# Kernel optimization log

Measured on AMD Instinct MI355X. Metric: run time of the kernel, lower is better.

## Reference

```python
import jax, jax.numpy as jnp
import numpy as np

N = 100_000      # nodes
E = 1_200_000    # edges (before self-loops)
F_IN = 128       # num_node_features
G = 256          # number of graphs in the batch
C = 10           # num_classes
NEG_SLOPE = 0.2  # PyG GATConv default


def setup_inputs() -> dict:
    key = jax.random.key(0)
    ks = jax.random.split(key, 20)
    x = jax.random.normal(ks[0], (N, F_IN), jnp.float32)
    edge_index = jax.random.randint(ks[1], (2, E), 0, N, dtype=jnp.int32)
    # sorted graph assignment covering all G graphs (no empty segments)
    batch = (jnp.arange(N, dtype=jnp.int32) * G) // N

    def lin(k, fi, fo):
        return jax.random.normal(k, (fi, fo), jnp.float32) * (1.0 / np.sqrt(fi))

    dims = [(F_IN, 16), (16, 32), (32, 64)]
    params = {}
    for i, (fi, fo) in enumerate(dims, start=1):
        params[f"W{i}"] = lin(ks[3 * i], fi, fo)
        params[f"a{i}_src"] = jax.random.normal(ks[3 * i + 1], (fo,), jnp.float32) * 0.1
        params[f"a{i}_dst"] = jax.random.normal(ks[3 * i + 2], (fo,), jnp.float32) * 0.1
        params[f"b{i}"] = jnp.zeros((fo,), jnp.float32)
    params["fc_w"] = lin(ks[15], 64, C)
    params["fc_b"] = jnp.zeros((C,), jnp.float32)
    return {"x": x, "edge_index": edge_index, "batch": batch, **params}


def _gat_layer(x, src, dst, W, a_src, a_dst, b):
    # h = Theta x; e_ij = LeakyReLU(a_src.h_j + a_dst.h_i), softmax over dst i
    h = x @ W                                     # [N, F]
    s = h @ a_src                                 # [N]
    d = h @ a_dst                                 # [N]
    logits = jax.nn.leaky_relu(s[src] + d[dst], NEG_SLOPE)   # [E+N]
    m = jax.ops.segment_max(logits, dst, num_segments=N)     # per-dst max
    ex = jnp.exp(logits - m[dst])
    denom = jax.ops.segment_sum(ex, dst, num_segments=N)
    alpha = ex / (denom[dst] + 1e-16)             # [E+N]
    out = jax.ops.segment_sum(alpha[:, None] * h[src], dst, num_segments=N)
    return out + b


def reference(x, edge_index, batch, W1, a1_src, a1_dst, b1, W2, a2_src, a2_dst, b2,
              W3, a3_src, a3_dst, b3, fc_w, fc_b):
    # add self-loops (PyG GATConv default) -> every dst segment non-empty
    loops = jnp.arange(N, dtype=edge_index.dtype)
    src = jnp.concatenate([edge_index[0], loops])
    dst = jnp.concatenate([edge_index[1], loops])

    h = jax.nn.relu(_gat_layer(x, src, dst, W1, a1_src, a1_dst, b1))
    # F.dropout(training=False) is a no-op in eval
    h = jax.nn.relu(_gat_layer(h, src, dst, W2, a2_src, a2_dst, b2))
    h = jax.nn.relu(_gat_layer(h, src, dst, W3, a3_src, a3_dst, b3))
    pooled = jax.ops.segment_max(h, batch, num_segments=G)   # global_max_pool [G, 64]
    logits = pooled @ fc_w + fc_b
    return jax.nn.log_softmax(logits, axis=1)
```

## Files before the change

kernel.cpp:

```cpp
#include <hip/hip_runtime.h>
#include <hip/hip_bf16.h>
#include <hip/hip_fp16.h>
#include <math.h>

#define NEG_SLOPE 0.2f
#define NCHUNK 1024
#define BSHIFT 8
#define BNODES 256

__device__ __forceinline__ float leaky(float x) { return x > 0.f ? x : NEG_SLOPE * x; }
__device__ __forceinline__ int usan(int v, int n) { return ((unsigned)v < (unsigned)n) ? v : 0; }

__global__ void chunk_hist(const int* __restrict__ dst, int E, int Ec, int nbuck,
                           int* __restrict__ hmatT) {
    extern __shared__ int hist[];
    int c = blockIdx.x;
    for (int b = threadIdx.x; b < nbuck; b += 256) hist[b] = 0;
    __syncthreads();
    int lo = c * Ec, hi = min(E, lo + Ec);
    for (int e = lo + threadIdx.x; e < hi; e += 256) atomicAdd(&hist[dst[e] >> BSHIFT], 1);
    __syncthreads();
    for (int b = threadIdx.x; b < nbuck; b += 256) hmatT[b * NCHUNK + c] = hist[b];
}

__global__ void mat_scan(int* __restrict__ hmatT, int* __restrict__ btot) {
    __shared__ int wsum[4];
    int b = blockIdx.x;
    int t = threadIdx.x;
    int lane = t & 63, wave = t >> 6;
    int base = b * NCHUNK + t * 4;
    int a0 = hmatT[base], a1 = hmatT[base + 1], a2 = hmatT[base + 2], a3 = hmatT[base + 3];
    int ts = a0 + a1 + a2 + a3;
    int incl = ts;
#pragma unroll
    for (int o = 1; o < 64; o <<= 1) {
        int v = __shfl_up(incl, o);
        if (lane >= o) incl += v;
    }
    if (lane == 63) wsum[wave] = incl;
    __syncthreads();
    int wadd = 0;
#pragma unroll
    for (int w = 0; w < 4; w++) if (w < wave) wadd += wsum[w];
    int excl = wadd + incl - ts;
    hmatT[base] = excl;
    hmatT[base + 1] = excl + a0;
    hmatT[base + 2] = excl + a0 + a1;
    hmatT[base + 3] = excl + a0 + a1 + a2;
    if (t == 255) btot[b] = wadd + incl;
}

__global__ void base_scan(const int* __restrict__ btot, int nbuck, int* __restrict__ bbase,
                          int* __restrict__ offs, int N, int E) {
    __shared__ int wsum[8];
    int t = threadIdx.x;
    int lane = t & 63, wave = t >> 6;
    int v = (t < nbuck) ? btot[t] : 0;
    int incl = v;
#pragma unroll
    for (int o = 1; o < 64; o <<= 1) {
        int s = __shfl_up(incl, o);
        if (lane >= o) incl += s;
    }
    if (lane == 63) wsum[wave] = incl;
    __syncthreads();
    int wadd = 0;
#pragma unroll
    for (int w = 0; w < 8; w++) if (w < wave) wadd += wsum[w];
    incl += wadd;
    if (t <= nbuck) bbase[t] = incl - v;
    if (t == 0) offs[N] = N + E;
}

__global__ void chunk_scatter(const int* __restrict__ src, const int* __restrict__ dst,
                              int E, int Ec, int nbuck, const int* __restrict__ hmatT,
                              const int* __restrict__ bbase, int* __restrict__ bbuf) {
    extern __shared__ int cur[];
    int c = blockIdx.x;
    for (int b = threadIdx.x; b < nbuck; b += 256) cur[b] = bbase[b] + hmatT[b * NCHUNK + c];
    __syncthreads();
    int lo = c * Ec, hi = min(E, lo + Ec);
    for (int e = lo + threadIdx.x; e < hi; e += 256) {
        int d = dst[e];
        int b = d >> BSHIFT;
        int p = atomicAdd(&cur[b], 1);
        bbuf[p] = (src[e] << BSHIFT) | (d & (BNODES - 1));
    }
}

__global__ void bucket_build(const int* __restrict__ bbase, const int* __restrict__ bbuf,
                             int N, int* __restrict__ offs, int* __restrict__ csr) {
    __shared__ int hist[BNODES];
    __shared__ int offl[BNODES];
    __shared__ int cur[BNODES];
    __shared__ int wsum[4];
    int b = blockIdx.x;
    int t = threadIdx.x;
    int lane = t & 63, wave = t >> 6;
    hist[t] = 0;
    __syncthreads();
    int lo = bbase[b], hi = bbase[b + 1];
    for (int j = lo + t; j < hi; j += BNODES) atomicAdd(&hist[bbuf[j] & (BNODES - 1)], 1);
    __syncthreads();
    int own = hist[t];
    int incl = own;
#pragma unroll
    for (int o = 1; o < 64; o <<= 1) {
        int s = __shfl_up(incl, o);
        if (lane >= o) incl += s;
    }
    if (lane == 63) wsum[wave] = incl;
    __syncthreads();
    int wadd = 0;
#pragma unroll
    for (int w = 0; w < 4; w++) if (w < wave) wadd += wsum[w];
    int excl = wadd + incl - own;
    int n = (b << BSHIFT) + t;
    int off_n = n + bbase[b] + excl;
    offl[t] = off_n;
    cur[t] = 0;
    if (n < N) {
        offs[n] = off_n;
        csr[off_n] = n;
    }
    __syncthreads();
    for (int j = lo + t; j < hi; j += BNODES) {
        int v = bbuf[j];
        int ld = v & (BNODES - 1);
        int r = atomicAdd(&cur[ld], 1);
        csr[offl[ld] + 1 + r] = v >> BSHIFT;
    }
}


template <int FIN, int FOUT>
__global__ void transform(const float* __restrict__ xin, const float* __restrict__ W,
                          const float* __restrict__ adst,
                          __half* __restrict__ h, float* __restrict__ dv, int N) {
    constexpr int TPN = FOUT / 4;
    constexpr int BN  = 256 / TPN;
    constexpr int PITCH = FIN + 4;
    __shared__ float xs[BN * PITCH];
    __shared__ float wl[FIN * FOUT];
    __shared__ float bl[FOUT];
    for (int j = threadIdx.x; j < FIN * FOUT; j += 256) wl[j] = W[j];
    if (threadIdx.x < FOUT) bl[threadIdx.x] = adst[threadIdx.x];
    int base = blockIdx.x * BN;
    constexpr int NV = BN * FIN / 4;
    const float4* xg = (const float4*)xin + (size_t)base * (FIN / 4);
    int limv = ((N - base) * FIN) >> 2;
    for (int v = threadIdx.x; v < NV; v += 256) {
        int n = v / (FIN / 4), c = v % (FIN / 4);
        float4 val = (v < limv) ? xg[v] : make_float4(0.f, 0.f, 0.f, 0.f);
        *(float4*)&xs[n * PITCH + c * 4] = val;
    }
    __syncthreads();
    int node_l = threadIdx.x / TPN;
    int fq = (threadIdx.x % TPN) * 4;
    int node = base + node_l;
    const float* xrow = &xs[node_l * PITCH];
    float4 acc = make_float4(0.f, 0.f, 0.f, 0.f);
#pragma unroll 8
    for (int k = 0; k < FIN; k++) {
        float xv = xrow[k];
        float4 w4 = *(const float4*)&wl[k * FOUT + fq];
        acc.x += xv * w4.x; acc.y += xv * w4.y; acc.z += xv * w4.z; acc.w += xv * w4.w;
    }
    if (node < N) {
        __half2* hp = (__half2*)(h + (size_t)node * FOUT + fq);
        hp[0] = __floats2half2_rn(acc.x, acc.y);
        hp[1] = __floats2half2_rn(acc.z, acc.w);
        float dp = acc.x * bl[fq] + acc.y * bl[fq + 1] + acc.z * bl[fq + 2] + acc.w * bl[fq + 3];
#pragma unroll
        for (int o = TPN / 2; o > 0; o >>= 1) dp += __shfl_xor(dp, o);
        if (fq == 0) dv[node] = dp;
    }
}


template <int FI, int FO>
__global__ void gat_trans(const __half* __restrict__ h, const float* __restrict__ asrc,
                          const float* __restrict__ dv, const int* __restrict__ offs,
                          const int* __restrict__ csr, const float* __restrict__ bias,
                          const float* __restrict__ Wn, const float* __restrict__ an_s,
                          const float* __restrict__ an_d,
                          __half* __restrict__ h2, float* __restrict__ sv2,
                          float* __restrict__ dv2, int N) {
    constexpr int L  = FI / 8;
    constexpr int L2 = 2 * L;
    constexpr int CPL = FO / L2;
    constexpr int NPB = 256 / L2;
    __shared__ float wl[FI * FO];
    __shared__ float al[FO], bl[FO];
    for (int j = threadIdx.x; j < FI * FO; j += 256) wl[j] = Wn[j];
    if (threadIdx.x < FO) { al[threadIdx.x] = an_s[threadIdx.x]; bl[threadIdx.x] = an_d[threadIdx.x]; }
    __syncthreads();
    int lane  = threadIdx.x % L;
    int lane2 = threadIdx.x % L2;
    int wlane = threadIdx.x & 63;
    int half  = (threadIdx.x / L) & 1;
    int grpbase = wlane & ~(L2 - 1);
    int i = blockIdx.x * NPB + threadIdx.x / L2;
    if (i >= N) return;
    float asr[8];
#pragma unroll
    for (int k = 0; k < 8; k++) asr[k] = asrc[lane * 8 + k];
    int beg = offs[i], end = offs[i + 1];
    float di = dv[i];
    float acc[8];
#pragma unroll
    for (int c = 0; c < 8; c++) acc[c] = 0.f;
    float ssum = 0.f;

    int j0 = beg + 4 * half;
    int j1 = j0 + 8;
    bool vA = (j0 + 4 <= end);
    bool vB = (j1 + 4 <= end);
    int j0e = vA ? j0 : beg;
    int a0 = usan(csr[j0e], N),     a1 = usan(csr[j0e + 1], N);
    int a2 = usan(csr[j0e + 2], N), a3 = usan(csr[j0e + 3], N);
    uint4 uA0 = *((const uint4*)(h + (size_t)a0 * FI) + lane);
    uint4 uA1 = *((const uint4*)(h + (size_t)a1 * FI) + lane);
    uint4 uA2 = *((const uint4*)(h + (size_t)a2 * FI) + lane);
    uint4 uA3 = *((const uint4*)(h + (size_t)a3 * FI) + lane);
    int j1e = vB ? j1 : beg;
    int b0 = usan(csr[j1e], N),     b1 = usan(csr[j1e + 1], N);
    int b2 = usan(csr[j1e + 2], N), b3 = usan(csr[j1e + 3], N);
    while (vA) {
        int j2 = j1 + 8;
        bool vC = vB && (j2 + 4 <= end);
        uint4 uB0 = *((const uint4*)(h + (size_t)b0 * FI) + lane);
        uint4 uB1 = *((const uint4*)(h + (size_t)b1 * FI) + lane);
        uint4 uB2 = *((const uint4*)(h + (size_t)b2 * FI) + lane);
        uint4 uB3 = *((const uint4*)(h + (size_t)b3 * FI) + lane);
        int j2e = vC ? j2 : beg;
        int c0 = usan(csr[j2e], N),     c1 = usan(csr[j2e + 1], N);
        int c2 = usan(csr[j2e + 2], N), c3 = usan(csr[j2e + 3], N);
        float2 f0[4], f1[4], f2[4], f3[4];
#pragma unroll
        for (int c = 0; c < 4; c++) {
            f0[c] = __half22float2(((const __half2*)&uA0)[c]);
            f1[c] = __half22float2(((const __half2*)&uA1)[c]);
            f2[c] = __half22float2(((const __half2*)&uA2)[c]);
            f3[c] = __half22float2(((const __half2*)&uA3)[c]);
        }
        float p0 = 0.f, p1 = 0.f, p2 = 0.f, p3 = 0.f;
#pragma unroll
        for (int c = 0; c < 4; c++) {
            p0 += f0[c].x * asr[2 * c] + f0[c].y * asr[2 * c + 1];
            p1 += f1[c].x * asr[2 * c] + f1[c].y * asr[2 * c + 1];
            p2 += f2[c].x * asr[2 * c] + f2[c].y * asr[2 * c + 1];
            p3 += f3[c].x * asr[2 * c] + f3[c].y * asr[2 * c + 1];
        }
#pragma unroll
        for (int o = 1; o < L; o <<= 1) {
            p0 += __shfl_xor(p0, o); p1 += __shfl_xor(p1, o);
            p2 += __shfl_xor(p2, o); p3 += __shfl_xor(p3, o);
        }
        float w0 = __expf(leaky(p0 + di));
        float w1 = __expf(leaky(p1 + di));
        float w2 = __expf(leaky(p2 + di));
        float w3 = __expf(leaky(p3 + di));
        ssum += (w0 + w1) + (w2 + w3);
#pragma unroll
        for (int c = 0; c < 4; c++) {
            acc[2 * c]     += w0 * f0[c].x + w1 * f1[c].x + w2 * f2[c].x + w3 * f3[c].x;
            acc[2 * c + 1] += w0 * f0[c].y + w1 * f1[c].y + w2 * f2[c].y + w3 * f3[c].y;
        }
        uA0 = uB0; uA1 = uB1; uA2 = uB2; uA3 = uB3;
        b0 = c0; b1 = c1; b2 = c2; b3 = c3;
        j0 = j1; j1 = j2; vA = vB; vB = vC;
    }
    int rem = end - j0;
    if (rem > 0) {
        int o1 = rem > 1 ? 1 : 0;
        int o2 = rem > 2 ? 2 : o1;
        int t0 = usan(csr[j0], N), t1 = usan(csr[j0 + o1], N), t2 = usan(csr[j0 + o2], N);
        uint4 r0 = *((const uint4*)(h + (size_t)t0 * FI) + lane);
        uint4 r1 = *((const uint4*)(h + (size_t)t1 * FI) + lane);
        uint4 r2 = *((const uint4*)(h + (size_t)t2 * FI) + lane);
        float2 g0[4], g1[4], g2[4];
#pragma unroll
        for (int c = 0; c < 4; c++) {
            g0[c] = __half22float2(((const __half2*)&r0)[c]);
            g1[c] = __half22float2(((const __half2*)&r1)[c]);
            g2[c] = __half22float2(((const __half2*)&r2)[c]);
        }
        float q0 = 0.f, q1 = 0.f, q2 = 0.f;
#pragma unroll
        for (int c = 0; c < 4; c++) {
            q0 += g0[c].x * asr[2 * c] + g0[c].y * asr[2 * c + 1];
            q1 += g1[c].x * asr[2 * c] + g1[c].y * asr[2 * c + 1];
            q2 += g2[c].x * asr[2 * c] + g2[c].y * asr[2 * c + 1];
        }
#pragma unroll
        for (int o = 1; o < L; o <<= 1) {
            q0 += __shfl_xor(q0, o); q1 += __shfl_xor(q1, o); q2 += __shfl_xor(q2, o);
        }
        float w0t = __expf(leaky(q0 + di));
        float w1t = rem > 1 ? __expf(leaky(q1 + di)) : 0.f;
        float w2t = rem > 2 ? __expf(leaky(q2 + di)) : 0.f;
        ssum += w0t + w1t + w2t;
#pragma unroll
        for (int c = 0; c < 4; c++) {
            acc[2 * c]     += w0t * g0[c].x + w1t * g1[c].x + w2t * g2[c].x;
            acc[2 * c + 1] += w0t * g0[c].y + w1t * g1[c].y + w2t * g2[c].y;
        }
    }
#pragma unroll
    for (int c = 0; c < 8; c++) acc[c] += __shfl_xor(acc[c], L);
    ssum += __shfl_xor(ssum, L);

    float inv = 1.0f / ssum;
    float4 ba = ((const float4*)bias)[lane * 2];
    float4 bb = ((const float4*)bias)[lane * 2 + 1];
    float yv[8];
    yv[0] = fmaxf(acc[0] * inv + ba.x, 0.f);
    yv[1] = fmaxf(acc[1] * inv + ba.y, 0.f);
    yv[2] = fmaxf(acc[2] * inv + ba.z, 0.f);
    yv[3] = fmaxf(acc[3] * inv + ba.w, 0.f);
    yv[4] = fmaxf(acc[4] * inv + bb.x, 0.f);
    yv[5] = fmaxf(acc[5] * inv + bb.y, 0.f);
    yv[6] = fmaxf(acc[6] * inv + bb.z, 0.f);
    yv[7] = fmaxf(acc[7] * inv + bb.w, 0.f);
    int colbase = lane2 * CPL;
    float oacc[CPL];
#pragma unroll
    for (int c = 0; c < CPL; c++) oacc[c] = 0.f;
#pragma unroll
    for (int jj = 0; jj < L; jj++) {
        float v[8];
#pragma unroll
        for (int r = 0; r < 8; r++) v[r] = __shfl(yv[r], grpbase + jj);
#pragma unroll
        for (int r = 0; r < 8; r++) {
            const float* wrow = &wl[(jj * 8 + r) * FO + colbase];
#pragma unroll
            for (int c = 0; c < CPL; c++) oacc[c] += v[r] * wrow[c];
        }
    }
    __half2 hp[CPL / 2];
#pragma unroll
    for (int c = 0; c < CPL / 2; c++) hp[c] = __floats2half2_rn(oacc[2 * c], oacc[2 * c + 1]);
    *((uint4*)(h2 + (size_t)i * FO + colbase)) = *(uint4*)&hp[0];
    float sp = 0.f, dp = 0.f;
#pragma unroll
    for (int c = 0; c < CPL; c++) { sp += oacc[c] * al[colbase + c]; dp += oacc[c] * bl[colbase + c]; }
#pragma unroll
    for (int o = 1; o < L2; o <<= 1) { sp += __shfl_xor(sp, o); dp += __shfl_xor(dp, o); }
    if (lane2 == 0) { sv2[i] = sp; dv2[i] = dp; }
}


template <int F>
__global__ void gat_fused(const __half* __restrict__ h, const float* __restrict__ sv,
                          const float* __restrict__ dv, const int* __restrict__ offs,
                          const int* __restrict__ csr, const float* __restrict__ bias,
                          __half* __restrict__ y, int N) {
    constexpr int L  = F / 8;
    constexpr int L2 = 2 * L;
    constexpr int NPB = 256 / L2;
    int lane  = threadIdx.x % L;
    int half  = (threadIdx.x / L) & 1;
    int wlane = threadIdx.x & 63;
    int sgbase = wlane & ~(L - 1);
    int i = blockIdx.x * NPB + threadIdx.x / L2;
    if (i >= N) return;
    int beg = offs[i], end = offs[i + 1];
    float di = dv[i];
    float acc[8];
#pragma unroll
    for (int c = 0; c < 8; c++) acc[c] = 0.f;
    float ssum = 0.f;
    const int k3 = lane & 3;

    int j0 = beg + 4 * half;
    int j1 = j0 + 8;
    bool vA = (j0 + 4 <= end);
    bool vB = (j1 + 4 <= end);
    int j0e = vA ? j0 : beg;
    int a0 = usan(csr[j0e], N),     a1 = usan(csr[j0e + 1], N);
    int a2 = usan(csr[j0e + 2], N), a3 = usan(csr[j0e + 3], N);
    uint4 uA0 = *((const uint4*)(h + (size_t)a0 * F) + lane);
    uint4 uA1 = *((const uint4*)(h + (size_t)a1 * F) + lane);
    uint4 uA2 = *((const uint4*)(h + (size_t)a2 * F) + lane);
    uint4 uA3 = *((const uint4*)(h + (size_t)a3 * F) + lane);
    int sel = a0;
    if (k3 == 1) sel = a1; else if (k3 == 2) sel = a2; else if (k3 == 3) sel = a3;
    float svA = sv[sel];
    int j1e = vB ? j1 : beg;
    int b0 = usan(csr[j1e], N),     b1 = usan(csr[j1e + 1], N);
    int b2 = usan(csr[j1e + 2], N), b3 = usan(csr[j1e + 3], N);
    while (vA) {
        int j2 = j1 + 8;
        bool vC = vB && (j2 + 4 <= end);
        uint4 uB0 = *((const uint4*)(h + (size_t)b0 * F) + lane);
        uint4 uB1 = *((const uint4*)(h + (size_t)b1 * F) + lane);
        uint4 uB2 = *((const uint4*)(h + (size_t)b2 * F) + lane);
        uint4 uB3 = *((const uint4*)(h + (size_t)b3 * F) + lane);
        int selB = b0;
        if (k3 == 1) selB = b1; else if (k3 == 2) selB = b2; else if (k3 == 3) selB = b3;
        float svB = sv[selB];
        int j2e = vC ? j2 : beg;
        int c0 = usan(csr[j2e], N),     c1 = usan(csr[j2e + 1], N);
        int c2 = usan(csr[j2e + 2], N), c3 = usan(csr[j2e + 3], N);
        float myw = __expf(leaky(svA + di));
        float w0 = __shfl(myw, sgbase + 0);
        float w1 = __shfl(myw, sgbase + 1);
        float w2 = __shfl(myw, sgbase + 2);
        float w3 = __shfl(myw, sgbase + 3);
        ssum += (w0 + w1) + (w2 + w3);
#pragma unroll
        for (int c = 0; c < 4; c++) {
            float2 f0 = __half22float2(((const __half2*)&uA0)[c]);
            float2 f1 = __half22float2(((const __half2*)&uA1)[c]);
            float2 f2 = __half22float2(((const __half2*)&uA2)[c]);
            float2 f3 = __half22float2(((const __half2*)&uA3)[c]);
            acc[2 * c]     += w0 * f0.x + w1 * f1.x + w2 * f2.x + w3 * f3.x;
            acc[2 * c + 1] += w0 * f0.y + w1 * f1.y + w2 * f2.y + w3 * f3.y;
        }
        uA0 = uB0; uA1 = uB1; uA2 = uB2; uA3 = uB3;
        svA = svB;
        b0 = c0; b1 = c1; b2 = c2; b3 = c3;
        j0 = j1; j1 = j2; vA = vB; vB = vC;
    }
    int rem = end - j0;
    if (rem > 0) {
        int o1 = rem > 1 ? 1 : 0;
        int o2 = rem > 2 ? 2 : o1;
        int t0 = usan(csr[j0], N), t1 = usan(csr[j0 + o1], N), t2 = usan(csr[j0 + o2], N);
        uint4 r0 = *((const uint4*)(h + (size_t)t0 * F) + lane);
        uint4 r1 = *((const uint4*)(h + (size_t)t1 * F) + lane);
        uint4 r2 = *((const uint4*)(h + (size_t)t2 * F) + lane);
        float s0 = sv[t0], s1 = sv[t1], s2 = sv[t2];
        float w0t = __expf(leaky(s0 + di));
        float w1t = rem > 1 ? __expf(leaky(s1 + di)) : 0.f;
        float w2t = rem > 2 ? __expf(leaky(s2 + di)) : 0.f;
        ssum += w0t + w1t + w2t;
#pragma unroll
        for (int c = 0; c < 4; c++) {
            float2 f0 = __half22float2(((const __half2*)&r0)[c]);
            float2 f1 = __half22float2(((const __half2*)&r1)[c]);
            float2 f2 = __half22float2(((const __half2*)&r2)[c]);
            acc[2 * c]     += w0t * f0.x + w1t * f1.x + w2t * f2.x;
            acc[2 * c + 1] += w0t * f0.y + w1t * f1.y + w2t * f2.y;
        }
    }
#pragma unroll
    for (int c = 0; c < 8; c++) acc[c] += __shfl_xor(acc[c], L);
    ssum += __shfl_xor(ssum, L);
    if (half == 0) {
        float inv = 1.0f / ssum;
        float4 ba = ((const float4*)bias)[lane * 2];
        float4 bb = ((const float4*)bias)[lane * 2 + 1];
        __half2 o[4];
        o[0] = __floats2half2_rn(fmaxf(acc[0] * inv + ba.x, 0.f), fmaxf(acc[1] * inv + ba.y, 0.f));
        o[1] = __floats2half2_rn(fmaxf(acc[2] * inv + ba.z, 0.f), fmaxf(acc[3] * inv + ba.w, 0.f));
        o[2] = __floats2half2_rn(fmaxf(acc[4] * inv + bb.x, 0.f), fmaxf(acc[5] * inv + bb.y, 0.f));
        o[3] = __floats2half2_rn(fmaxf(acc[6] * inv + bb.z, 0.f), fmaxf(acc[7] * inv + bb.w, 0.f));
        ((uint4*)(y + (size_t)i * F))[lane] = *(uint4*)&o[0];
    }
}


__global__ void pool_head(const __half* __restrict__ y, const float* __restrict__ fcw,
                          const float* __restrict__ fcb, float* __restrict__ out,
                          int N, int G, int C) {
    __shared__ float red[256];
    __shared__ float pl[64];
    int g = blockIdx.x;
    long long gl = g;
    int start = (int)((gl * N + G - 1) / G);
    int end = (int)(((gl + 1) * N + G - 1) / G);
    int f = threadIdx.x & 63, w = threadIdx.x >> 6;
    float m = 0.f;
    for (int i = start + w; i < end; i += 4) m = fmaxf(m, __half2float(y[(size_t)i * 64 + f]));
    red[threadIdx.x] = m;
    __syncthreads();
    if (threadIdx.x < 64) {
        pl[f] = fmaxf(fmaxf(red[f], red[64 + f]), fmaxf(red[128 + f], red[192 + f]));
    }
    __syncthreads();
    if (threadIdx.x < 64) {
        int c = threadIdx.x;
        float z = -1e30f;
        if (c < C) {
            z = fcb[c];
            for (int k = 0; k < 64; k++) z += pl[k] * fcw[k * 10 + c];
        }
        float zm = z;
#pragma unroll
        for (int o = 1; o < 16; o <<= 1) zm = fmaxf(zm, __shfl_xor(zm, o));
        float e = (c < C) ? __expf(z - zm) : 0.f;
        float se = e;
#pragma unroll
        for (int o = 1; o < 16; o <<= 1) se += __shfl_xor(se, o);
        if (c < C) out[g * C + c] = z - zm - logf(se);
    }
}


extern "C" void kernel_launch(void* const* d_in, const int* in_sizes, int n_in,
                              void* d_out, int out_size, void* d_ws, size_t ws_size,
                              hipStream_t stream) {
    const float* x    = (const float*)d_in[0];
    const int*   eidx = (const int*)d_in[1];
    const float* W1 = (const float*)d_in[3];
    const float* a1s = (const float*)d_in[4];
    const float* a1d = (const float*)d_in[5];
    const float* b1 = (const float*)d_in[6];
    const float* W2 = (const float*)d_in[7];
    const float* a2s = (const float*)d_in[8];
    const float* a2d = (const float*)d_in[9];
    const float* b2 = (const float*)d_in[10];
    const float* W3 = (const float*)d_in[11];
    const float* a3s = (const float*)d_in[12];
    const float* a3d = (const float*)d_in[13];
    const float* b3 = (const float*)d_in[14];
    const float* fcw = (const float*)d_in[15];
    const float* fcb = (const float*)d_in[16];
    float* out = (float*)d_out;

    const int N = in_sizes[2];
    const int E = in_sizes[1] / 2;
    const int C = in_sizes[16];
    const int G = out_size / C;

    const int* src = eidx;
    const int* dst = eidx + E;

    size_t off = 0;
    auto alloc = [&](size_t bytes) -> void* {
        void* p = (char*)d_ws + off;
        off += (bytes + 255) & ~(size_t)255;
        return p;
    };
    int* offs   = (int*)alloc((size_t)(N + 1) * 4);
    int* csr    = (int*)alloc((size_t)(E + N) * 4 + 256);
    float* sbufA = (float*)alloc((size_t)N * 4);
    float* dbufA = (float*)alloc((size_t)N * 4);
    float* sbufB = (float*)alloc((size_t)N * 4);
    float* dbufB = (float*)alloc((size_t)N * 4);
    __half* hA = (__half*)alloc((size_t)N * 64 * 2);
    __half* hB = (__half*)alloc((size_t)N * 64 * 2);

    const int NBUCK = (N + BNODES - 1) >> BSHIFT;
    const int Ec = (E + NCHUNK - 1) / NCHUNK;
    int* hmatT = (int*)alloc((size_t)NBUCK * NCHUNK * 4);
    int* btot  = (int*)alloc((size_t)NBUCK * 4);
    int* bbase = (int*)alloc((size_t)(NBUCK + 1) * 4);
    int* bbuf  = (int*)hB;

    const size_t histBytes = (size_t)NBUCK * 4;

    chunk_hist<<<NCHUNK, 256, histBytes, stream>>>(dst, E, Ec, NBUCK, hmatT);
    mat_scan<<<NBUCK, 256, 0, stream>>>(hmatT, btot);
    base_scan<<<1, 512, 0, stream>>>(btot, NBUCK, bbase, offs, N, E);
    chunk_scatter<<<NCHUNK, 256, histBytes, stream>>>(src, dst, E, Ec, NBUCK, hmatT, bbase, bbuf);
    bucket_build<<<NBUCK, BNODES, 0, stream>>>(bbase, bbuf, N, offs, csr);

    transform<128, 16><<<(N + 63) / 64, 256, 0, stream>>>(x, W1, a1d, hA, dbufA, N);
    gat_trans<16, 32><<<(N + 63) / 64, 256, 0, stream>>>(hA, a1s, dbufA, offs, csr, b1,
                                                         W2, a2s, a2d, hB, sbufB, dbufB, N);
    gat_trans<32, 64><<<(N + 31) / 32, 256, 0, stream>>>(hB, a2s, dbufB, offs, csr, b2,
                                                         W3, a3s, a3d, hA, sbufA, dbufA, N);
    gat_fused<64><<<(N + 15) / 16, 256, 0, stream>>>(hA, sbufA, dbufA, offs, csr, b3, hB, N);

    pool_head<<<G, 256, 0, stream>>>(hB, fcw, fcb, out, N, G, C);
}
```

Baseline: 272.2 us.

## Sort nodes by in-degree to balance per-wave work in GAT aggregation kernels

```diff
diff --git a/kernel.cpp b/kernel.cpp
--- a/kernel.cpp
+++ b/kernel.cpp
@@ -51,7 +51,7 @@
 }
 
 __global__ void base_scan(const int* __restrict__ btot, int nbuck, int* __restrict__ bbase,
-                          int* __restrict__ offs, int N, int E) {
+                          int* __restrict__ offs, int N, int E, int* __restrict__ dhist) {
     __shared__ int wsum[8];
     int t = threadIdx.x;
     int lane = t & 63, wave = t >> 6;
@@ -70,6 +70,7 @@
     incl += wadd;
     if (t <= nbuck) bbase[t] = incl - v;
     if (t == 0) offs[N] = N + E;
+    if (t < 256) dhist[t] = 0;
 }
 
 __global__ void chunk_scatter(const int* __restrict__ src, const int* __restrict__ dst,
@@ -129,6 +130,50 @@
         int ld = v & (BNODES - 1);
         int r = atomicAdd(&cur[ld], 1);
         csr[offl[ld] + 1 + r] = v >> BSHIFT;
+    }
+}
+
+
+__global__ void deg_hist(const int* __restrict__ offs, int N, int* __restrict__ dhist) {
+    __shared__ int lh[256];
+    int t = threadIdx.x;
+    lh[t] = 0;
+    __syncthreads();
+    int i = blockIdx.x * 256 + t;
+    if (i < N) {
+        int d = min(offs[i + 1] - offs[i], 255);
+        atomicAdd(&lh[d], 1);
+    }
+    __syncthreads();
+    if (lh[t]) atomicAdd(&dhist[t], lh[t]);
+}
+
+__global__ void deg_scan(const int* __restrict__ dhist, int* __restrict__ dcur) {
+    __shared__ int wsum[4];
+    int t = threadIdx.x;
+    int lane = t & 63, wave = t >> 6;
+    int v = dhist[t];
+    int incl = v;
+#pragma unroll
+    for (int o = 1; o < 64; o <<= 1) {
+        int s = __shfl_up(incl, o);
+        if (lane >= o) incl += s;
+    }
+    if (lane == 63) wsum[wave] = incl;
+    __syncthreads();
+    int wadd = 0;
+#pragma unroll
+    for (int w = 0; w < 4; w++) if (w < wave) wadd += wsum[w];
+    dcur[t] = wadd + incl - v;
+}
+
+__global__ void deg_scatter(const int* __restrict__ offs, int N, int* __restrict__ dcur,
+                            int* __restrict__ order) {
+    int i = blockIdx.x * 256 + threadIdx.x;
+    if (i < N) {
+        int d = min(offs[i + 1] - offs[i], 255);
+        int p = atomicAdd(&dcur[d], 1);
+        order[p] = i;
     }
 }
 
@@ -181,7 +226,8 @@
 template <int FI, int FO>
 __global__ void gat_trans(const __half* __restrict__ h, const float* __restrict__ asrc,
                           const float* __restrict__ dv, const int* __restrict__ offs,
-                          const int* __restrict__ csr, const float* __restrict__ bias,
+                          const int* __restrict__ csr, const int* __restrict__ order,
+                          const float* __restrict__ bias,
                           const float* __restrict__ Wn, const float* __restrict__ an_s,
                           const float* __restrict__ an_d,
                           __half* __restrict__ h2, float* __restrict__ sv2,
@@ -200,8 +246,9 @@
     int wlane = threadIdx.x & 63;
     int half  = (threadIdx.x / L) & 1;
     int grpbase = wlane & ~(L2 - 1);
-    int i = blockIdx.x * NPB + threadIdx.x / L2;
-    if (i >= N) return;
+    int idx = blockIdx.x * NPB + threadIdx.x / L2;
+    if (idx >= N) return;
+    int i = order[idx];
     float asr[8];
 #pragma unroll
     for (int k = 0; k < 8; k++) asr[k] = asrc[lane * 8 + k];
@@ -355,7 +402,8 @@
 template <int F>
 __global__ void gat_fused(const __half* __restrict__ h, const float* __restrict__ sv,
                           const float* __restrict__ dv, const int* __restrict__ offs,
-                          const int* __restrict__ csr, const float* __restrict__ bias,
+                          const int* __restrict__ csr, const int* __restrict__ order,
+                          const float* __restrict__ bias,
                           __half* __restrict__ y, int N) {
     constexpr int L  = F / 8;
     constexpr int L2 = 2 * L;
@@ -364,8 +412,9 @@
     int half  = (threadIdx.x / L) & 1;
     int wlane = threadIdx.x & 63;
     int sgbase = wlane & ~(L - 1);
-    int i = blockIdx.x * NPB + threadIdx.x / L2;
-    if (i >= N) return;
+    int idx = blockIdx.x * NPB + threadIdx.x / L2;
+    if (idx >= N) return;
+    int i = order[idx];
     int beg = offs[i], end = offs[i + 1];
     float di = dv[i];
     float acc[8];
@@ -537,6 +586,9 @@
     };
     int* offs   = (int*)alloc((size_t)(N + 1) * 4);
     int* csr    = (int*)alloc((size_t)(E + N) * 4 + 256);
+    int* order  = (int*)alloc((size_t)N * 4);
+    int* dhist  = (int*)alloc(256 * 4);
+    int* dcur   = (int*)alloc(256 * 4);
     float* sbufA = (float*)alloc((size_t)N * 4);
     float* dbufA = (float*)alloc((size_t)N * 4);
     float* sbufB = (float*)alloc((size_t)N * 4);
@@ -555,16 +607,21 @@
 
     chunk_hist<<<NCHUNK, 256, histBytes, stream>>>(dst, E, Ec, NBUCK, hmatT);
     mat_scan<<<NBUCK, 256, 0, stream>>>(hmatT, btot);
-    base_scan<<<1, 512, 0, stream>>>(btot, NBUCK, bbase, offs, N, E);
+    base_scan<<<1, 512, 0, stream>>>(btot, NBUCK, bbase, offs, N, E, dhist);
     chunk_scatter<<<NCHUNK, 256, histBytes, stream>>>(src, dst, E, Ec, NBUCK, hmatT, bbase, bbuf);
     bucket_build<<<NBUCK, BNODES, 0, stream>>>(bbase, bbuf, N, offs, csr);
 
+    const int NB256 = (N + 255) / 256;
+    deg_hist<<<NB256, 256, 0, stream>>>(offs, N, dhist);
+    deg_scan<<<1, 256, 0, stream>>>(dhist, dcur);
+    deg_scatter<<<NB256, 256, 0, stream>>>(offs, N, dcur, order);
+
     transform<128, 16><<<(N + 63) / 64, 256, 0, stream>>>(x, W1, a1d, hA, dbufA, N);
-    gat_trans<16, 32><<<(N + 63) / 64, 256, 0, stream>>>(hA, a1s, dbufA, offs, csr, b1,
+    gat_trans<16, 32><<<(N + 63) / 64, 256, 0, stream>>>(hA, a1s, dbufA, offs, csr, order, b1,
                                                          W2, a2s, a2d, hB, sbufB, dbufB, N);
-    gat_trans<32, 64><<<(N + 31) / 32, 256, 0, stream>>>(hB, a2s, dbufB, offs, csr, b2,
+    gat_trans<32, 64><<<(N + 31) / 32, 256, 0, stream>>>(hB, a2s, dbufB, offs, csr, order, b2,
                                                          W3, a3s, a3d, hA, sbufA, dbufA, N);
-    gat_fused<64><<<(N + 15) / 16, 256, 0, stream>>>(hA, sbufA, dbufA, offs, csr, b3, hB, N);
+    gat_fused<64><<<(N + 15) / 16, 256, 0, stream>>>(hA, sbufA, dbufA, offs, csr, order, b3, hB, N);
 
     pool_head<<<G, 256, 0, stream>>>(hB, fcw, fcb, out, N, G, C);
 }
```

After: 595.0 us. +118.6%, slower.
